# Optimization experiments

Measured on AMD Instinct MI355X. Metric: run time of the kernel, lower is better.

Reference implementation:

```python
import jax, jax.numpy as jnp
import numpy as np

B, S, I, H = 1024, 512, 1, 50  # batch, seq_len, input_size, hidden_size


def setup_inputs() -> dict:
    key = jax.random.key(0)
    ks = jax.random.split(key, 7)
    s_ih = 1.0 / np.sqrt(H)
    return {
        "x": jax.random.normal(ks[0], (B, S, I), dtype=jnp.float32),
        "h0": jnp.zeros((1, B, H), dtype=jnp.float32),
        "c0": jnp.zeros((1, B, H), dtype=jnp.float32),
        # PyTorch nn.LSTM params, gate order [i, f, g, o]
        "W_ih": jax.random.uniform(ks[1], (4 * H, I), jnp.float32, -s_ih, s_ih),
        "W_hh": jax.random.uniform(ks[2], (4 * H, H), jnp.float32, -s_ih, s_ih),
        "b_ih": jax.random.uniform(ks[3], (4 * H,), jnp.float32, -s_ih, s_ih),
        "b_hh": jax.random.uniform(ks[4], (4 * H,), jnp.float32, -s_ih, s_ih),
        "fc_w": jax.random.uniform(ks[5], (1, H), jnp.float32, -s_ih, s_ih),
        "fc_b": jax.random.uniform(ks[6], (1,), jnp.float32, -s_ih, s_ih),
    }


def reference(x, h0, c0, W_ih, W_hh, b_ih, b_hh, fc_w, fc_b):
    # Precompute the input projection for all timesteps: [B, S, 4H] -> scan over S
    x_proj = jnp.einsum("bsi,gi->bsg", x, W_ih) + (b_ih + b_hh)
    x_proj = jnp.transpose(x_proj, (1, 0, 2))  # [S, B, 4H]

    def step(carry, xp_t):
        h, c = carry  # each [B, H]
        gates = xp_t + h @ W_hh.T  # [B, 4H]
        i_g, f_g, g_g, o_g = jnp.split(gates, 4, axis=-1)
        c_new = jax.nn.sigmoid(f_g) * c + jax.nn.sigmoid(i_g) * jnp.tanh(g_g)
        h_new = jax.nn.sigmoid(o_g) * jnp.tanh(c_new)
        return (h_new, c_new), None

    (h_n, c_n), _ = jax.lax.scan(step, (h0[0], c0[0]), x_proj)
    # out[:, -1, :] is the final hidden state; fc head: [B, H] -> [B, 1]
    out = h_n @ fc_w.T + fc_b
    return out, h_n[None], c_n[None]
```

## Files before the change

### kernel.cpp

```cpp
#include <hip/hip_runtime.h>


typedef _Float16 half2v __attribute__((ext_vector_type(2)));

#define LOG2E 1.44269504088896340736f
#define B_ 1024
#define S_ 512
#define H_ 50

__device__ __forceinline__ float rcp_(float x) { return __builtin_amdgcn_rcpf(x); }
__device__ __forceinline__ float ex2_(float x) { return __builtin_amdgcn_exp2f(x); }

__global__ void lstm_pack(const float* __restrict__ W_ih, const float* __restrict__ W_hh,
                          const float* __restrict__ b_ih, const float* __restrict__ b_hh,
                          unsigned* __restrict__ wpk, float* __restrict__ wih_pk,
                          float* __restrict__ bias_pk)
{
    int tid = blockIdx.x * blockDim.x + threadIdx.x;
    int stride = blockDim.x * gridDim.x;
    for (int p = tid; p < 4 * 25 * 64; p += stride) {
        int j = p & 63;
        int m = (p >> 6) % 25;
        int g = p / (25 * 64);
        float s = (g == 2) ? (2.0f * LOG2E) : (-LOG2E);
        float a = 0.0f, bb = 0.0f;
        if (j < H_) {
            int row = g * H_ + j;
            a  = s * W_hh[row * H_ + 2 * m];
            bb = s * W_hh[row * H_ + 2 * m + 1];
        }
        half2v hv;
        hv.x = (_Float16)a;
        hv.y = (_Float16)bb;
        wpk[p] = __builtin_bit_cast(unsigned, hv);
    }
    for (int p = tid; p < 4 * 64; p += stride) {
        int j = p & 63;
        int g = p >> 6;
        float s = (g == 2) ? (2.0f * LOG2E) : (-LOG2E);
        float wi = 0.0f, bb = 0.0f;
        if (j < H_) {
            int row = g * H_ + j;
            wi = s * W_ih[row];
            bb = s * (b_ih[row] + b_hh[row]);
        }
        wih_pk[p] = wi;
        bias_pk[p] = bb;
    }
}

__global__ __launch_bounds__(64) void lstm_main(
    const float* __restrict__ x, const float* __restrict__ h0, const float* __restrict__ c0,
    const float* __restrict__ fc_w, const float* __restrict__ fc_b,
    const unsigned* __restrict__ wpk, const float* __restrict__ wih_pk,
    const float* __restrict__ bias_pk, float* __restrict__ out)
{
    const int b = blockIdx.x;
    const int j = threadIdx.x;

    __shared__ float xs[S_];
    #pragma unroll
    for (int t = 0; t < S_ / 64; ++t) xs[j + 64 * t] = x[b * S_ + 64 * t + j];

    half2v w0[25], w1[25], w2[25], w3[25];
    #pragma unroll
    for (int m = 0; m < 25; ++m) {
        w0[m] = __builtin_bit_cast(half2v, wpk[(0 * 25 + m) * 64 + j]);
        w1[m] = __builtin_bit_cast(half2v, wpk[(1 * 25 + m) * 64 + j]);
        w2[m] = __builtin_bit_cast(half2v, wpk[(2 * 25 + m) * 64 + j]);
        w3[m] = __builtin_bit_cast(half2v, wpk[(3 * 25 + m) * 64 + j]);
    }
    float wih0 = wih_pk[0 * 64 + j], wih1 = wih_pk[1 * 64 + j];
    float wih2 = wih_pk[2 * 64 + j], wih3 = wih_pk[3 * 64 + j];
    float bs0 = bias_pk[0 * 64 + j], bs1 = bias_pk[1 * 64 + j];
    float bs2 = bias_pk[2 * 64 + j], bs3 = bias_pk[3 * 64 + j];

    float h = (j < H_) ? h0[b * H_ + j] : 0.0f;
    float c = (j < H_) ? c0[b * H_ + j] : 0.0f;

    __syncthreads();

    float hn = __shfl_down(h, 1);
    unsigned hpk = __builtin_bit_cast(unsigned, __builtin_amdgcn_cvt_pkrtz(h, hn));

    for (int s = 0; s < S_; ++s) {
        float xt = xs[s];
        float aA0 = __builtin_fmaf(xt, wih0, bs0);
        float aA1 = __builtin_fmaf(xt, wih1, bs1);
        float aA2 = __builtin_fmaf(xt, wih2, bs2);
        float aA3 = __builtin_fmaf(xt, wih3, bs3);
        float aB0 = 0.0f, aB1 = 0.0f, aB2 = 0.0f, aB3 = 0.0f;

        #pragma unroll
        for (int m = 0; m < 25; ++m) {
            unsigned um = (unsigned)__builtin_amdgcn_readlane((int)hpk, 2 * m);
            half2v hm = __builtin_bit_cast(half2v, um);
            if (m & 1) {
                aB0 = __builtin_amdgcn_fdot2(hm, w0[m], aB0, false);
                aB1 = __builtin_amdgcn_fdot2(hm, w1[m], aB1, false);
                aB2 = __builtin_amdgcn_fdot2(hm, w2[m], aB2, false);
                aB3 = __builtin_amdgcn_fdot2(hm, w3[m], aB3, false);
            } else {
                aA0 = __builtin_amdgcn_fdot2(hm, w0[m], aA0, false);
                aA1 = __builtin_amdgcn_fdot2(hm, w1[m], aA1, false);
                aA2 = __builtin_amdgcn_fdot2(hm, w2[m], aA2, false);
                aA3 = __builtin_amdgcn_fdot2(hm, w3[m], aA3, false);
            }
        }
        float a0 = aA0 + aB0;
        float a1 = aA1 + aB1;
        float a2 = aA2 + aB2;
        float a3 = aA3 + aB3;

        float ei = ex2_(a0); float si = rcp_(1.0f + ei);
        float ef = ex2_(a1); float sf = rcp_(1.0f + ef);
        float eg = ex2_(a2);
        float tg = __builtin_fmaf(-2.0f, rcp_(1.0f + eg), 1.0f);
        float eo = ex2_(a3); float so = rcp_(1.0f + eo);

        c = __builtin_fmaf(sf, c, si * tg);
        float ec = ex2_((2.0f * LOG2E) * c);
        float tc = __builtin_fmaf(-2.0f, rcp_(1.0f + ec), 1.0f);
        h = so * tc;

        float hnn = __shfl_down(h, 1);
        hpk = __builtin_bit_cast(unsigned, __builtin_amdgcn_cvt_pkrtz(h, hnn));
    }

    if (j < H_) {
        out[B_ + b * H_ + j]            = h;
        out[B_ + B_ * H_ + b * H_ + j]  = c;
    }
    float p = (j < H_) ? h * fc_w[j] : 0.0f;
    #pragma unroll
    for (int off = 32; off > 0; off >>= 1) p += __shfl_xor(p, off);
    if (j == 0) out[b] = p + fc_b[0];
}

extern "C" void kernel_launch(void* const* d_in, const int* in_sizes, int n_in,
                              void* d_out, int out_size, void* d_ws, size_t ws_size,
                              hipStream_t stream)
{
    const float* x    = (const float*)d_in[0];
    const float* h0   = (const float*)d_in[1];
    const float* c0   = (const float*)d_in[2];
    const float* W_ih = (const float*)d_in[3];
    const float* W_hh = (const float*)d_in[4];
    const float* b_ih = (const float*)d_in[5];
    const float* b_hh = (const float*)d_in[6];
    const float* fc_w = (const float*)d_in[7];
    const float* fc_b = (const float*)d_in[8];
    float* out = (float*)d_out;

    unsigned* wpk  = (unsigned*)d_ws;
    float* wih_pk  = (float*)((char*)d_ws + 6400 * 4);
    float* bias_pk = (float*)((char*)d_ws + 6400 * 4 + 256 * 4);

    lstm_pack<<<16, 256, 0, stream>>>(W_ih, W_hh, b_ih, b_hh, wpk, wih_pk, bias_pk);
    lstm_main<<<B_, 64, 0, stream>>>(x, h0, c0, fc_w, fc_b, wpk, wih_pk, bias_pk, out);
}
```

Measured before the change: 202.4 us.

## Switch recurrent matvec from fp16 dot2 to fp32 FMA with LDS broadcast

```diff
diff --git a/kernel.cpp b/kernel.cpp
--- a/kernel.cpp
+++ b/kernel.cpp
@@ -1,7 +1,5 @@
 #include <hip/hip_runtime.h>
 
-
-typedef _Float16 half2v __attribute__((ext_vector_type(2)));
 
 #define LOG2E 1.44269504088896340736f
 #define B_ 1024
@@ -13,26 +11,19 @@
 
 __global__ void lstm_pack(const float* __restrict__ W_ih, const float* __restrict__ W_hh,
                           const float* __restrict__ b_ih, const float* __restrict__ b_hh,
-                          unsigned* __restrict__ wpk, float* __restrict__ wih_pk,
+                          float* __restrict__ wf, float* __restrict__ wih_pk,
                           float* __restrict__ bias_pk)
 {
     int tid = blockIdx.x * blockDim.x + threadIdx.x;
     int stride = blockDim.x * gridDim.x;
-    for (int p = tid; p < 4 * 25 * 64; p += stride) {
+    for (int p = tid; p < 4 * H_ * 64; p += stride) {
         int j = p & 63;
-        int m = (p >> 6) % 25;
-        int g = p / (25 * 64);
+        int m = (p >> 6) % H_;
+        int g = p / (H_ * 64);
         float s = (g == 2) ? (2.0f * LOG2E) : (-LOG2E);
-        float a = 0.0f, bb = 0.0f;
-        if (j < H_) {
-            int row = g * H_ + j;
-            a  = s * W_hh[row * H_ + 2 * m];
-            bb = s * W_hh[row * H_ + 2 * m + 1];
-        }
-        half2v hv;
-        hv.x = (_Float16)a;
-        hv.y = (_Float16)bb;
-        wpk[p] = __builtin_bit_cast(unsigned, hv);
+        float a = 0.0f;
+        if (j < H_) a = s * W_hh[(g * H_ + j) * H_ + m];
+        wf[p] = a;
     }
     for (int p = tid; p < 4 * 64; p += stride) {
         int j = p & 63;
@@ -49,68 +40,81 @@
     }
 }
 
-__global__ __launch_bounds__(64) void lstm_main(
-    const float* __restrict__ x, const float* __restrict__ h0, const float* __restrict__ c0,
-    const float* __restrict__ fc_w, const float* __restrict__ fc_b,
-    const unsigned* __restrict__ wpk, const float* __restrict__ wih_pk,
-    const float* __restrict__ bias_pk, float* __restrict__ out)
+__global__ __launch_bounds__(64)
+__attribute__((amdgpu_waves_per_eu(1, 1)))
+void lstm_main(const float* __restrict__ x, const float* __restrict__ h0,
+               const float* __restrict__ c0, const float* __restrict__ fc_w,
+               const float* __restrict__ fc_b, const float* __restrict__ wf,
+               const float* __restrict__ wih_pk, const float* __restrict__ bias_pk,
+               float* __restrict__ out)
 {
     const int b = blockIdx.x;
     const int j = threadIdx.x;
 
-    __shared__ float xs[S_];
+    __shared__ float hs[64];
+
+    float w0[H_], w1[H_], w2[H_], w3[H_];
     #pragma unroll
-    for (int t = 0; t < S_ / 64; ++t) xs[j + 64 * t] = x[b * S_ + 64 * t + j];
+    for (int m = 0; m < H_; ++m) {
+        w0[m] = wf[(0 * H_ + m) * 64 + j];
+        w1[m] = wf[(1 * H_ + m) * 64 + j];
+        w2[m] = wf[(2 * H_ + m) * 64 + j];
+        w3[m] = wf[(3 * H_ + m) * 64 + j];
+    }
+    #pragma unroll
+    for (int m = 0; m < H_; ++m) {
+        asm volatile("" : "+v"(w0[m]));
+        asm volatile("" : "+v"(w1[m]));
+        asm volatile("" : "+v"(w2[m]));
+        asm volatile("" : "+v"(w3[m]));
+    }
 
-    half2v w0[25], w1[25], w2[25], w3[25];
-    #pragma unroll
-    for (int m = 0; m < 25; ++m) {
-        w0[m] = __builtin_bit_cast(half2v, wpk[(0 * 25 + m) * 64 + j]);
-        w1[m] = __builtin_bit_cast(half2v, wpk[(1 * 25 + m) * 64 + j]);
-        w2[m] = __builtin_bit_cast(half2v, wpk[(2 * 25 + m) * 64 + j]);
-        w3[m] = __builtin_bit_cast(half2v, wpk[(3 * 25 + m) * 64 + j]);
-    }
     float wih0 = wih_pk[0 * 64 + j], wih1 = wih_pk[1 * 64 + j];
     float wih2 = wih_pk[2 * 64 + j], wih3 = wih_pk[3 * 64 + j];
     float bs0 = bias_pk[0 * 64 + j], bs1 = bias_pk[1 * 64 + j];
     float bs2 = bias_pk[2 * 64 + j], bs3 = bias_pk[3 * 64 + j];
+    asm volatile("" : "+v"(wih0), "+v"(wih1), "+v"(wih2), "+v"(wih3),
+                      "+v"(bs0), "+v"(bs1), "+v"(bs2), "+v"(bs3));
 
     float h = (j < H_) ? h0[b * H_ + j] : 0.0f;
     float c = (j < H_) ? c0[b * H_ + j] : 0.0f;
+    hs[j] = h;
 
-    __syncthreads();
-
-    float hn = __shfl_down(h, 1);
-    unsigned hpk = __builtin_bit_cast(unsigned, __builtin_amdgcn_cvt_pkrtz(h, hn));
+    const float* __restrict__ xrow = x + b * S_;
+    float xt = xrow[0];
 
     for (int s = 0; s < S_; ++s) {
-        float xt = xs[s];
-        float aA0 = __builtin_fmaf(xt, wih0, bs0);
-        float aA1 = __builtin_fmaf(xt, wih1, bs1);
-        float aA2 = __builtin_fmaf(xt, wih2, bs2);
-        float aA3 = __builtin_fmaf(xt, wih3, bs3);
-        float aB0 = 0.0f, aB1 = 0.0f, aB2 = 0.0f, aB3 = 0.0f;
+        int sn = s + 1 < S_ ? s + 1 : S_ - 1;
+        float xt_n = xrow[sn];
+
+        float hp[H_];
+        #pragma unroll
+        for (int m = 0; m < H_ / 2; ++m) {
+            float2 t = *reinterpret_cast<const float2*>(&hs[2 * m]);
+            hp[2 * m]     = t.x;
+            hp[2 * m + 1] = t.y;
+        }
+
+        float a0A = __builtin_fmaf(xt, wih0, bs0), a0B = 0.0f;
+        float a1A = __builtin_fmaf(xt, wih1, bs1), a1B = 0.0f;
+        float a2A = __builtin_fmaf(xt, wih2, bs2), a2B = 0.0f;
+        float a3A = __builtin_fmaf(xt, wih3, bs3), a3B = 0.0f;
 
         #pragma unroll
-        for (int m = 0; m < 25; ++m) {
-            unsigned um = (unsigned)__builtin_amdgcn_readlane((int)hpk, 2 * m);
-            half2v hm = __builtin_bit_cast(half2v, um);
-            if (m & 1) {
-                aB0 = __builtin_amdgcn_fdot2(hm, w0[m], aB0, false);
-                aB1 = __builtin_amdgcn_fdot2(hm, w1[m], aB1, false);
-                aB2 = __builtin_amdgcn_fdot2(hm, w2[m], aB2, false);
-                aB3 = __builtin_amdgcn_fdot2(hm, w3[m], aB3, false);
-            } else {
-                aA0 = __builtin_amdgcn_fdot2(hm, w0[m], aA0, false);
-                aA1 = __builtin_amdgcn_fdot2(hm, w1[m], aA1, false);
-                aA2 = __builtin_amdgcn_fdot2(hm, w2[m], aA2, false);
-                aA3 = __builtin_amdgcn_fdot2(hm, w3[m], aA3, false);
-            }
+        for (int k = 0; k < H_; k += 2) {
+            a0A = __builtin_fmaf(hp[k], w0[k], a0A);
+            a1A = __builtin_fmaf(hp[k], w1[k], a1A);
+            a2A = __builtin_fmaf(hp[k], w2[k], a2A);
+            a3A = __builtin_fmaf(hp[k], w3[k], a3A);
+            a0B = __builtin_fmaf(hp[k + 1], w0[k + 1], a0B);
+            a1B = __builtin_fmaf(hp[k + 1], w1[k + 1], a1B);
+            a2B = __builtin_fmaf(hp[k + 1], w2[k + 1], a2B);
+            a3B = __builtin_fmaf(hp[k + 1], w3[k + 1], a3B);
         }
-        float a0 = aA0 + aB0;
-        float a1 = aA1 + aB1;
-        float a2 = aA2 + aB2;
-        float a3 = aA3 + aB3;
+        float a0 = a0A + a0B;
+        float a1 = a1A + a1B;
+        float a2 = a2A + a2B;
+        float a3 = a3A + a3B;
 
         float ei = ex2_(a0); float si = rcp_(1.0f + ei);
         float ef = ex2_(a1); float sf = rcp_(1.0f + ef);
@@ -123,8 +127,8 @@
         float tc = __builtin_fmaf(-2.0f, rcp_(1.0f + ec), 1.0f);
         h = so * tc;
 
-        float hnn = __shfl_down(h, 1);
-        hpk = __builtin_bit_cast(unsigned, __builtin_amdgcn_cvt_pkrtz(h, hnn));
+        hs[j] = h;
+        xt = xt_n;
     }
 
     if (j < H_) {
@@ -152,10 +156,10 @@
     const float* fc_b = (const float*)d_in[8];
     float* out = (float*)d_out;
 
-    unsigned* wpk  = (unsigned*)d_ws;
-    float* wih_pk  = (float*)((char*)d_ws + 6400 * 4);
-    float* bias_pk = (float*)((char*)d_ws + 6400 * 4 + 256 * 4);
+    float* wf      = (float*)d_ws;
+    float* wih_pk  = (float*)((char*)d_ws + 12800 * 4);
+    float* bias_pk = (float*)((char*)d_ws + 12800 * 4 + 256 * 4);
 
-    lstm_pack<<<16, 256, 0, stream>>>(W_ih, W_hh, b_ih, b_hh, wpk, wih_pk, bias_pk);
-    lstm_main<<<B_, 64, 0, stream>>>(x, h0, c0, fc_w, fc_b, wpk, wih_pk, bias_pk, out);
+    lstm_pack<<<16, 256, 0, stream>>>(W_ih, W_hh, b_ih, b_hh, wf, wih_pk, bias_pk);
+    lstm_main<<<B_, 64, 0, stream>>>(x, h0, c0, fc_w, fc_b, wf, wih_pk, bias_pk, out);
 }
```

Result: no change. 201.9 us (-0.3%).
